# Kernel tuning notes

Measured on AMD Instinct MI355X. Metric: run time of the kernel, lower is better.

Reference implementation:

```python
import jax, jax.numpy as jnp
import numpy as np

# Norse LIFParameters defaults (method='super', alpha=100)
DT = 1e-3
TAU_SYN_INV = 200.0   # 1/5e-3
TAU_MEM_INV = 100.0   # 1/1e-2
V_TH = 1.0
V_LEAK = 0.0
V_RESET = 0.0
ALPHA = 100.0
T = 40                # ConstantCurrentLIFEncoder(40)
SCALE = 50.0
HIDDEN = 64


@jax.custom_vjp
def super_spike(x):
    # Heaviside forward, SuperSpike surrogate gradient backward
    return (x > 0).astype(x.dtype)

def _ss_fwd(x):
    return super_spike(x), x

def _ss_bwd(x, g):
    return (g / (ALPHA * jnp.abs(x) + 1.0) ** 2,)

super_spike.defvjp(_ss_fwd, _ss_bwd)


def encode(current):
    """norse lif_current_encoder unrolled T steps with constant current.
    current: (B, F) -> spikes (T, B, F). Elementwise, so all four encoder
    calls of the original are fused by concatenating along features."""
    def step(v, _):
        v = v + DT * TAU_MEM_INV * ((V_LEAK - v) + current)
        z = super_spike(v - V_TH)
        v = v - z * (v - V_RESET)
        return v, z
    _, spikes = jax.lax.scan(step, jnp.zeros_like(current), None, length=T)
    return spikes


def lif_step(x, z, v, i, w_in, w_rec):
    # norse lif_step semantics
    i_dec = i - DT * TAU_SYN_INV * i
    v_dec = v + DT * TAU_MEM_INV * ((V_LEAK - v) + i)
    z_new = super_spike(v_dec - V_TH)
    v_new = (1.0 - z_new) * v_dec + z_new * V_RESET
    i_new = i_dec + x @ w_in.T + z @ w_rec.T
    return z_new, v_new, i_new


def li_step(x, v, i, w_in):
    # norse li_step (leaky integrator readout)
    i_dec = i - DT * TAU_SYN_INV * i
    v_new = v + DT * TAU_MEM_INV * ((V_LEAK - v) + i)
    i_new = i_dec + x @ w_in.T
    return v_new, i_new


def setup_inputs() -> dict:
    key = jax.random.key(0)
    ks = jax.random.split(key, 9)
    B, S, A = 16384, 24, 4
    def w(k, out_d, in_d):
        return jax.random.normal(k, (out_d, in_d), jnp.float32) * np.sqrt(2.0 / in_d)
    return {
        "state": jax.random.normal(ks[0], (B, S), jnp.float32),
        "action": jax.random.normal(ks[1], (B, A), jnp.float32),
        "W_s_in": w(ks[2], HIDDEN, 2 * S),
        "W_s_rec": w(ks[3], HIDDEN, HIDDEN),
        "W_a_in": w(ks[4], HIDDEN, 2 * A),
        "W_a_rec": w(ks[5], HIDDEN, HIDDEN),
        "W_c_in": w(ks[6], HIDDEN, 2 * HIDDEN),
        "W_c_rec": w(ks[7], HIDDEN, HIDDEN),
        "W_ro": w(ks[8], 1, HIDDEN),
    }


def reference(state, action, W_s_in, W_s_rec, W_a_in, W_a_rec, W_c_in, W_c_rec, W_ro):
    B, S = state.shape
    # constant-current LIF encoding of pos/neg rectified state & action (fused)
    cur = jnp.concatenate([
        jax.nn.relu(SCALE * state), jax.nn.relu(-SCALE * state),
        jax.nn.relu(SCALE * action), jax.nn.relu(-SCALE * action)], axis=1)
    enc = encode(cur)                      # (T, B, 2S+2A)
    state_enc = enc[:, :, :2 * S]          # (T, B, 2S)
    action_enc = enc[:, :, 2 * S:]         # (T, B, 2A)

    z0 = jnp.zeros((B, HIDDEN), state.dtype)
    carry0 = (z0, z0, z0, jnp.zeros((B, 1), state.dtype), jnp.zeros((B, 1), state.dtype))

    def step(carry, xs):
        z, v, i, vli, ili = carry
        xs_s, xs_a = xs
        # NB: original shares one state s0 across all three LIF cells per step
        z_s, v, i = lif_step(xs_s, z, v, i, W_s_in, W_s_rec)
        z_a, v, i = lif_step(xs_a, z_s, v, i, W_a_in, W_a_rec)
        com = jnp.concatenate([z_s, z_a], axis=1)  # (B, 128)
        z, v, i = lif_step(com, z_a, v, i, W_c_in, W_c_rec)
        vli, ili = li_step(z, vli, ili, W_ro)
        return (z, v, i, vli, ili), vli

    _, voltages = jax.lax.scan(step, carry0, (state_enc, action_enc))  # (T, B, 1)
    return jnp.max(voltages, axis=0)  # (B, 1)
```

## Files before the change

kernel.cpp:

```cpp
#include <hip/hip_runtime.h>
#include <stdint.h>


typedef int   i32x4 __attribute__((ext_vector_type(4)));
typedef float f32x4 __attribute__((ext_vector_type(4)));

__launch_bounds__(256)
__attribute__((amdgpu_waves_per_eu(2, 2)))
__global__ void snn_main(const float* __restrict__ state, const float* __restrict__ action,
                         const float* __restrict__ Wsin, const float* __restrict__ Wsrec,
                         const float* __restrict__ Wain, const float* __restrict__ Warec,
                         const float* __restrict__ Wcin, const float* __restrict__ Wcrec,
                         const float* __restrict__ Wro, float* __restrict__ out) {
    __shared__ __align__(16) char smem[32768];

    const int tid  = threadIdx.x;
    const int lane = tid & 63, h = tid >> 6;
    const int l15  = lane & 15, g = lane >> 4;
    const int s    = l15 & 7;

    auto quant = [](float w, int* d) {
        float x = w * 0x1p25f;
        int d3 = __float2int_rn(x * 0x1p-21f); x -= (float)d3 * 0x1p21f;
        int d2 = __float2int_rn(x * 0x1p-14f); x -= (float)d2 * 0x1p14f;
        int d1 = __float2int_rn(x * 0x1p-7f);  x -= (float)d1 * 0x1p7f;
        int d0 = __float2int_rn(x);
        d[0] = d0; d[1] = d1; d[2] = d2; d[3] = d3;
    };
    auto quantMat = [&](auto src) {
        for (int i4 = tid; i4 < 2048; i4 += 256) {
            int base = i4 * 4; int n = base >> 7, k0 = base & 127;
            int sw = n * 128 + ((((k0 >> 4) ^ (n & 7)) << 4) | (k0 & 15));
            uint32_t pk[4] = {0u, 0u, 0u, 0u};
            #pragma unroll
            for (int e = 0; e < 4; ++e) {
                int d[4]; quant(src(n, k0 + e), d);
                #pragma unroll
                for (int p = 0; p < 4; ++p) pk[p] |= (uint32_t)(uint8_t)(char)d[p] << (8 * e);
            }
            #pragma unroll
            for (int p = 0; p < 4; ++p) *(uint32_t*)(smem + p * 8192 + sw) = pk[p];
        }
    };

    const int cS0 = ((g ^ s) << 4);
    const int cS1 = (((4 + g) ^ s) << 4);
    const int i1c = 5 + g;
    const int cC0 = (((1 + g) ^ s) << 4);
    const int cC1 = (((i1c & 8) | ((i1c & 7) ^ s)) << 4);

    i32x4 AS[4][2], AA[4][2], AC[4][2];
    const int arow = (h * 16 + l15) * 128;

    quantMat([&](int n, int k) -> float {
        if (k < 48)  return Wsin[n * 48 + k];
        if (k < 112) return Wsrec[n * 64 + (k - 48)];
        return 0.f;
    });
    __syncthreads();
    #pragma unroll
    for (int p = 0; p < 4; ++p)
    #pragma unroll
    for (int kt = 0; kt < 2; ++kt)
        AS[p][kt] = *(const i32x4*)(smem + p * 8192 + arow + (kt ? cS1 : cS0));
    __syncthreads();

    quantMat([&](int n, int k) -> float {
        float w = Wcin[n * 128 + k];
        if (k >= 64) w += Wcrec[n * 64 + (k - 64)];
        return w;
    });
    __syncthreads();
    #pragma unroll
    for (int p = 0; p < 4; ++p)
    #pragma unroll
    for (int kt = 0; kt < 2; ++kt)
        AC[p][kt] = *(const i32x4*)(smem + p * 8192 + arow + (kt ? cS1 : cS0));
    __syncthreads();

    quantMat([&](int n, int k) -> float {
        if (k < 8)              return Wain[n * 8 + k];
        if (k >= 16 && k < 80)  return Warec[n * 64 + (k - 16)];
        return 0.f;
    });
    __syncthreads();
    #pragma unroll
    for (int p = 0; p < 4; ++p)
    #pragma unroll
    for (int kt = 0; kt < 2; ++kt)
        AA[p][kt] = *(const i32x4*)(smem + p * 8192 + arow + (kt ? cS1 : cS0));
    __syncthreads();

    char*  bS    = smem;
    char*  bAC0  = smem + 2048;
    float* part0 = (float*)(smem + 10240);

    const int ixZs = 1 + h, ixZa = 5 + h, ixZc = 3 + h;
    const int zsOff = l15 * 256 + (((ixZs & 8) | ((ixZs & 7) ^ s)) << 4) + 4 * g;
    const int zaOff = l15 * 256 + (((ixZa & 8) | ((ixZa & 7) ^ s)) << 4) + 4 * g;
    const int zcOff = l15 * 128 + ((ixZc ^ s) << 4) + 4 * g;
    const int encOffS = l15 * 128 + ((h ^ s) << 4) + 4 * g;
    const int encOffA = l15 * 256 + (s << 4) + 4 * g;

    const int rowBase = blockIdx.x * 16;
    const int row = rowBase + l15;

    float cur[4], venc[4];
    #pragma unroll
    for (int e = 0; e < 4; ++e) {
        int f = h * 16 + 4 * g + e;
        float c = 0.f;
        if (f < 24)      c = fmaxf( 50.f * state[row * 24 + f], 0.f);
        else if (f < 48) c = fmaxf(-50.f * state[row * 24 + f - 24], 0.f);
        else if (f < 52) c = fmaxf( 50.f * action[row * 4 + f - 48], 0.f);
        else if (f < 56) c = fmaxf(-50.f * action[row * 4 + f - 52], 0.f);
        cur[e] = c; venc[e] = 0.f;
    }

    float wrof[4];
    #pragma unroll
    for (int r = 0; r < 4; ++r) wrof[r] = Wro[h * 16 + 4 * g + r];

    f32x4 v4 = (f32x4){0.f,0.f,0.f,0.f}, ic4 = (f32x4){0.f,0.f,0.f,0.f};
    bool zc[4] = {false, false, false, false};
    float vli = 0.f, ili = 0.f, vmax = 0.f;

    for (int t = 0; t < 40; ++t) {
        char*  bAC  = bAC0 + ((t & 1) << 12);
        float* part = part0 + ((t & 1) << 6);

        {
            uint32_t zw = (zc[0]?1u:0u)|(zc[1]?0x100u:0u)|(zc[2]?0x10000u:0u)|(zc[3]?0x1000000u:0u);
            *(uint32_t*)(bS + zcOff) = zw;
        }

        f32x4 vd = v4 + 0.1f * (ic4 - v4);
        bool zs[4];
        #pragma unroll
        for (int r = 0; r < 4; ++r) { zs[r] = (vd[r] - 1.0f) > 0.f; if (zs[r]) vd[r] = 0.f; }
        f32x4 vs = vd;
        {
            uint32_t zw = (zs[0]?1u:0u)|(zs[1]?0x100u:0u)|(zs[2]?0x10000u:0u)|(zs[3]?0x1000000u:0u);
            *(uint32_t*)(bAC + zsOff) = zw;
        }

        {
            uint32_t wrd = 0;
            #pragma unroll
            for (int e = 0; e < 4; ++e) {
                float vn = venc[e] + 0.1f * (cur[e] - venc[e]);
                bool sp = (vn - 1.0f) > 0.f;
                venc[e] = sp ? 0.f : vn;
                wrd |= sp ? (1u << (8 * e)) : 0u;
            }
            if (h < 3)          *(uint32_t*)(bS + encOffS) = wrd;
            else if (g < 2)     *(uint32_t*)(bAC + encOffA) = wrd;
        }

        __syncthreads();

        i32x4 acc[4];
        #pragma unroll
        for (int p = 0; p < 4; ++p) acc[p] = (i32x4){0,0,0,0};
        #pragma unroll
        for (int kt = 0; kt < 2; ++kt) {
            i32x4 b = *(const i32x4*)(bS + l15 * 128 + (kt ? cS1 : cS0));
            #pragma unroll
            for (int p = 0; p < 4; ++p)
                acc[p] = __builtin_amdgcn_mfma_i32_16x16x64_i8(AS[p][kt], b, acc[p], 0, 0, 0);
        }
        f32x4 icS;
        {
            i32x4 hi = acc[3] * 128 + acc[2];
            i32x4 lo = acc[1] * 128 + acc[0];
            f32x4 idec = ic4 - 0.2f * ic4;
            #pragma unroll
            for (int r = 0; r < 4; ++r)
                icS[r] = fmaf((float)lo[r], 0x1p-25f, fmaf((float)hi[r], 0x1p-11f, idec[r]));
        }

        vd = vs + 0.1f * (icS - vs);
        bool za[4];
        #pragma unroll
        for (int r = 0; r < 4; ++r) { za[r] = (vd[r] - 1.0f) > 0.f; if (za[r]) vd[r] = 0.f; }
        f32x4 va = vd;
        {
            uint32_t zw = (za[0]?1u:0u)|(za[1]?0x100u:0u)|(za[2]?0x10000u:0u)|(za[3]?0x1000000u:0u);
            *(uint32_t*)(bAC + zaOff) = zw;
        }

        #pragma unroll
        for (int p = 0; p < 4; ++p) acc[p] = (i32x4){0,0,0,0};
        #pragma unroll
        for (int kt = 0; kt < 2; ++kt) {
            i32x4 b = *(const i32x4*)(bAC + l15 * 256 + (kt ? cS1 : cS0));
            #pragma unroll
            for (int p = 0; p < 4; ++p)
                acc[p] = __builtin_amdgcn_mfma_i32_16x16x64_i8(AA[p][kt], b, acc[p], 0, 0, 0);
        }
        f32x4 icA;
        {
            i32x4 hi = acc[3] * 128 + acc[2];
            i32x4 lo = acc[1] * 128 + acc[0];
            f32x4 idec = icS - 0.2f * icS;
            #pragma unroll
            for (int r = 0; r < 4; ++r)
                icA[r] = fmaf((float)lo[r], 0x1p-25f, fmaf((float)hi[r], 0x1p-11f, idec[r]));
        }

        vd = va + 0.1f * (icA - va);
        #pragma unroll
        for (int r = 0; r < 4; ++r) { zc[r] = (vd[r] - 1.0f) > 0.f; if (zc[r]) vd[r] = 0.f; }
        v4 = vd;

        {
            float pr = 0.f;
            #pragma unroll
            for (int r = 0; r < 4; ++r) pr += zc[r] ? wrof[r] : 0.f;
            pr += __shfl_xor(pr, 16);
            pr += __shfl_xor(pr, 32);
            if (g == 0) part[h * 16 + l15] = pr;
        }

        __syncthreads();

        #pragma unroll
        for (int p = 0; p < 4; ++p) acc[p] = (i32x4){0,0,0,0};
        #pragma unroll
        for (int kt = 0; kt < 2; ++kt) {
            i32x4 b = *(const i32x4*)(bAC + l15 * 256 + (kt ? cC1 : cC0));
            #pragma unroll
            for (int p = 0; p < 4; ++p)
                acc[p] = __builtin_amdgcn_mfma_i32_16x16x64_i8(AC[p][kt], b, acc[p], 0, 0, 0);
        }
        {
            i32x4 hi = acc[3] * 128 + acc[2];
            i32x4 lo = acc[1] * 128 + acc[0];
            f32x4 idec = icA - 0.2f * icA;
            #pragma unroll
            for (int r = 0; r < 4; ++r)
                ic4[r] = fmaf((float)lo[r], 0x1p-25f, fmaf((float)hi[r], 0x1p-11f, idec[r]));
        }

        float pt = part[l15] + part[16 + l15] + part[32 + l15] + part[48 + l15];
        float vnew = vli + 0.1f * (ili - vli);
        ili = (ili - 0.2f * ili) + pt;
        vli = vnew;
        vmax = fmaxf(vmax, vli);
    }

    if (h == 0 && g == 0) out[rowBase + l15] = vmax;
}

extern "C" void kernel_launch(void* const* d_in, const int* in_sizes, int n_in,
                              void* d_out, int out_size, void* d_ws, size_t ws_size,
                              hipStream_t stream) {
    const float* state  = (const float*)d_in[0];
    const float* action = (const float*)d_in[1];
    const float* Wsin   = (const float*)d_in[2];
    const float* Wsrec  = (const float*)d_in[3];
    const float* Wain   = (const float*)d_in[4];
    const float* Warec  = (const float*)d_in[5];
    const float* Wcin   = (const float*)d_in[6];
    const float* Wcrec  = (const float*)d_in[7];
    const float* Wro    = (const float*)d_in[8];
    float* out = (float*)d_out;

    const int B = in_sizes[0] / 24;
    snn_main<<<B / 16, 256, 0, stream>>>(state, action, Wsin, Wsrec, Wain, Warec,
                                         Wcin, Wcrec, Wro, out);
}
```

Baseline: 208.2 us.

## Process two 16-row batch groups per block to amortize weight setup and barriers

Each block now handles 32 batch rows as two interleaved 16-row groups. Each group gets its own shared-memory spike buffers and partial-sum slots, and the per-step MFMA chains for the two groups are interleaved. This halves the number of blocks, which amortizes the per-block weight quantization and register loading and halves the barriers per row. The two independent groups also give the MFMA pipeline independent work to overlap. In exchange it raises register pressure under the fixed waves-per-EU setting, doubles shared memory use, and leaves fewer blocks to spread across CUs.

```diff
diff --git a/kernel.cpp b/kernel.cpp
--- a/kernel.cpp
+++ b/kernel.cpp
@@ -91,9 +91,9 @@
         AA[p][kt] = *(const i32x4*)(smem + p * 8192 + arow + (kt ? cS1 : cS0));
     __syncthreads();
 
-    char*  bS    = smem;
-    char*  bAC0  = smem + 2048;
-    float* part0 = (float*)(smem + 10240);
+    char*  bS_[2]  = { smem,        smem + 2048 };
+    char*  bACb[2] = { smem + 4096, smem + 12288 };
+    float* part0   = (float*)(smem + 20480);
 
     const int ixZs = 1 + h, ixZa = 5 + h, ixZc = 3 + h;
     const int zsOff = l15 * 256 + (((ixZs & 8) | ((ixZs & 7) ^ s)) << 4) + 4 * g;
@@ -102,154 +102,170 @@
     const int encOffS = l15 * 128 + ((h ^ s) << 4) + 4 * g;
     const int encOffA = l15 * 256 + (s << 4) + 4 * g;
 
-    const int rowBase = blockIdx.x * 16;
-    const int row = rowBase + l15;
-
-    float cur[4], venc[4];
+    const int rowBase = blockIdx.x * 32;
+
+    float cur[2][4], venc[2][4];
+    #pragma unroll
+    for (int gr = 0; gr < 2; ++gr)
     #pragma unroll
     for (int e = 0; e < 4; ++e) {
         int f = h * 16 + 4 * g + e;
+        int row = rowBase + gr * 16 + l15;
         float c = 0.f;
         if (f < 24)      c = fmaxf( 50.f * state[row * 24 + f], 0.f);
         else if (f < 48) c = fmaxf(-50.f * state[row * 24 + f - 24], 0.f);
         else if (f < 52) c = fmaxf( 50.f * action[row * 4 + f - 48], 0.f);
         else if (f < 56) c = fmaxf(-50.f * action[row * 4 + f - 52], 0.f);
-        cur[e] = c; venc[e] = 0.f;
+        cur[gr][e] = c; venc[gr][e] = 0.f;
     }
 
     float wrof[4];
     #pragma unroll
     for (int r = 0; r < 4; ++r) wrof[r] = Wro[h * 16 + 4 * g + r];
 
-    f32x4 v4 = (f32x4){0.f,0.f,0.f,0.f}, ic4 = (f32x4){0.f,0.f,0.f,0.f};
-    bool zc[4] = {false, false, false, false};
-    float vli = 0.f, ili = 0.f, vmax = 0.f;
+    f32x4 v4[2], ic4[2];
+    bool zc[2][4];
+    float vli[2], ili[2], vmax[2];
+    #pragma unroll
+    for (int gr = 0; gr < 2; ++gr) {
+        v4[gr] = (f32x4){0.f,0.f,0.f,0.f}; ic4[gr] = (f32x4){0.f,0.f,0.f,0.f};
+        vli[gr] = 0.f; ili[gr] = 0.f; vmax[gr] = 0.f;
+        #pragma unroll
+        for (int r = 0; r < 4; ++r) zc[gr][r] = false;
+    }
 
     for (int t = 0; t < 40; ++t) {
-        char*  bAC  = bAC0 + ((t & 1) << 12);
-        float* part = part0 + ((t & 1) << 6);
-
-        {
-            uint32_t zw = (zc[0]?1u:0u)|(zc[1]?0x100u:0u)|(zc[2]?0x10000u:0u)|(zc[3]?0x1000000u:0u);
-            *(uint32_t*)(bS + zcOff) = zw;
-        }
-
-        f32x4 vd = v4 + 0.1f * (ic4 - v4);
-        bool zs[4];
-        #pragma unroll
-        for (int r = 0; r < 4; ++r) { zs[r] = (vd[r] - 1.0f) > 0.f; if (zs[r]) vd[r] = 0.f; }
-        f32x4 vs = vd;
-        {
-            uint32_t zw = (zs[0]?1u:0u)|(zs[1]?0x100u:0u)|(zs[2]?0x10000u:0u)|(zs[3]?0x1000000u:0u);
-            *(uint32_t*)(bAC + zsOff) = zw;
-        }
-
-        {
+        char* bAC[2] = { bACb[0] + ((t & 1) << 12), bACb[1] + ((t & 1) << 12) };
+        float* part  = part0 + ((t & 1) << 7);
+
+        f32x4 vs[2], va[2], icS[2], icA[2];
+        bool zs[2][4], za[2][4];
+
+        #pragma unroll
+        for (int gr = 0; gr < 2; ++gr) {
+            uint32_t zw = (zc[gr][0]?1u:0u)|(zc[gr][1]?0x100u:0u)|(zc[gr][2]?0x10000u:0u)|(zc[gr][3]?0x1000000u:0u);
+            *(uint32_t*)(bS_[gr] + zcOff) = zw;
+
+            f32x4 vd = v4[gr] + 0.1f * (ic4[gr] - v4[gr]);
+            #pragma unroll
+            for (int r = 0; r < 4; ++r) { zs[gr][r] = (vd[r] - 1.0f) > 0.f; if (zs[gr][r]) vd[r] = 0.f; }
+            vs[gr] = vd;
+            uint32_t zw2 = (zs[gr][0]?1u:0u)|(zs[gr][1]?0x100u:0u)|(zs[gr][2]?0x10000u:0u)|(zs[gr][3]?0x1000000u:0u);
+            *(uint32_t*)(bAC[gr] + zsOff) = zw2;
+
             uint32_t wrd = 0;
             #pragma unroll
             for (int e = 0; e < 4; ++e) {
-                float vn = venc[e] + 0.1f * (cur[e] - venc[e]);
+                float vn = venc[gr][e] + 0.1f * (cur[gr][e] - venc[gr][e]);
                 bool sp = (vn - 1.0f) > 0.f;
-                venc[e] = sp ? 0.f : vn;
+                venc[gr][e] = sp ? 0.f : vn;
                 wrd |= sp ? (1u << (8 * e)) : 0u;
             }
-            if (h < 3)          *(uint32_t*)(bS + encOffS) = wrd;
-            else if (g < 2)     *(uint32_t*)(bAC + encOffA) = wrd;
+            if (h < 3)          *(uint32_t*)(bS_[gr] + encOffS) = wrd;
+            else if (g < 2)     *(uint32_t*)(bAC[gr] + encOffA) = wrd;
         }
 
         __syncthreads();
 
-        i32x4 acc[4];
-        #pragma unroll
-        for (int p = 0; p < 4; ++p) acc[p] = (i32x4){0,0,0,0};
-        #pragma unroll
-        for (int kt = 0; kt < 2; ++kt) {
-            i32x4 b = *(const i32x4*)(bS + l15 * 128 + (kt ? cS1 : cS0));
-            #pragma unroll
-            for (int p = 0; p < 4; ++p)
-                acc[p] = __builtin_amdgcn_mfma_i32_16x16x64_i8(AS[p][kt], b, acc[p], 0, 0, 0);
-        }
-        f32x4 icS;
-        {
+        #pragma unroll
+        for (int gr = 0; gr < 2; ++gr) {
+            i32x4 acc[4];
+            #pragma unroll
+            for (int p = 0; p < 4; ++p) acc[p] = (i32x4){0,0,0,0};
+            #pragma unroll
+            for (int kt = 0; kt < 2; ++kt) {
+                i32x4 b = *(const i32x4*)(bS_[gr] + l15 * 128 + (kt ? cS1 : cS0));
+                #pragma unroll
+                for (int p = 0; p < 4; ++p)
+                    acc[p] = __builtin_amdgcn_mfma_i32_16x16x64_i8(AS[p][kt], b, acc[p], 0, 0, 0);
+            }
             i32x4 hi = acc[3] * 128 + acc[2];
             i32x4 lo = acc[1] * 128 + acc[0];
-            f32x4 idec = ic4 - 0.2f * ic4;
+            f32x4 idec = ic4[gr] - 0.2f * ic4[gr];
             #pragma unroll
             for (int r = 0; r < 4; ++r)
-                icS[r] = fmaf((float)lo[r], 0x1p-25f, fmaf((float)hi[r], 0x1p-11f, idec[r]));
-        }
-
-        vd = vs + 0.1f * (icS - vs);
-        bool za[4];
-        #pragma unroll
-        for (int r = 0; r < 4; ++r) { za[r] = (vd[r] - 1.0f) > 0.f; if (za[r]) vd[r] = 0.f; }
-        f32x4 va = vd;
-        {
-            uint32_t zw = (za[0]?1u:0u)|(za[1]?0x100u:0u)|(za[2]?0x10000u:0u)|(za[3]?0x1000000u:0u);
-            *(uint32_t*)(bAC + zaOff) = zw;
-        }
-
-        #pragma unroll
-        for (int p = 0; p < 4; ++p) acc[p] = (i32x4){0,0,0,0};
-        #pragma unroll
-        for (int kt = 0; kt < 2; ++kt) {
-            i32x4 b = *(const i32x4*)(bAC + l15 * 256 + (kt ? cS1 : cS0));
-            #pragma unroll
-            for (int p = 0; p < 4; ++p)
-                acc[p] = __builtin_amdgcn_mfma_i32_16x16x64_i8(AA[p][kt], b, acc[p], 0, 0, 0);
-        }
-        f32x4 icA;
-        {
+                icS[gr][r] = fmaf((float)lo[r], 0x1p-25f, fmaf((float)hi[r], 0x1p-11f, idec[r]));
+        }
+
+        #pragma unroll
+        for (int gr = 0; gr < 2; ++gr) {
+            f32x4 vd = vs[gr] + 0.1f * (icS[gr] - vs[gr]);
+            #pragma unroll
+            for (int r = 0; r < 4; ++r) { za[gr][r] = (vd[r] - 1.0f) > 0.f; if (za[gr][r]) vd[r] = 0.f; }
+            va[gr] = vd;
+            uint32_t zw = (za[gr][0]?1u:0u)|(za[gr][1]?0x100u:0u)|(za[gr][2]?0x10000u:0u)|(za[gr][3]?0x1000000u:0u);
+            *(uint32_t*)(bAC[gr] + zaOff) = zw;
+        }
+
+        #pragma unroll
+        for (int gr = 0; gr < 2; ++gr) {
+            i32x4 acc[4];
+            #pragma unroll
+            for (int p = 0; p < 4; ++p) acc[p] = (i32x4){0,0,0,0};
+            #pragma unroll
+            for (int kt = 0; kt < 2; ++kt) {
+                i32x4 b = *(const i32x4*)(bAC[gr] + l15 * 256 + (kt ? cS1 : cS0));
+                #pragma unroll
+                for (int p = 0; p < 4; ++p)
+                    acc[p] = __builtin_amdgcn_mfma_i32_16x16x64_i8(AA[p][kt], b, acc[p], 0, 0, 0);
+            }
             i32x4 hi = acc[3] * 128 + acc[2];
             i32x4 lo = acc[1] * 128 + acc[0];
-            f32x4 idec = icS - 0.2f * icS;
+            f32x4 idec = icS[gr] - 0.2f * icS[gr];
             #pragma unroll
             for (int r = 0; r < 4; ++r)
-                icA[r] = fmaf((float)lo[r], 0x1p-25f, fmaf((float)hi[r], 0x1p-11f, idec[r]));
-        }
-
-        vd = va + 0.1f * (icA - va);
-        #pragma unroll
-        for (int r = 0; r < 4; ++r) { zc[r] = (vd[r] - 1.0f) > 0.f; if (zc[r]) vd[r] = 0.f; }
-        v4 = vd;
-
-        {
+                icA[gr][r] = fmaf((float)lo[r], 0x1p-25f, fmaf((float)hi[r], 0x1p-11f, idec[r]));
+        }
+
+        #pragma unroll
+        for (int gr = 0; gr < 2; ++gr) {
+            f32x4 vd = va[gr] + 0.1f * (icA[gr] - va[gr]);
+            #pragma unroll
+            for (int r = 0; r < 4; ++r) { zc[gr][r] = (vd[r] - 1.0f) > 0.f; if (zc[gr][r]) vd[r] = 0.f; }
+            v4[gr] = vd;
+
             float pr = 0.f;
             #pragma unroll
-            for (int r = 0; r < 4; ++r) pr += zc[r] ? wrof[r] : 0.f;
+            for (int r = 0; r < 4; ++r) pr += zc[gr][r] ? wrof[r] : 0.f;
             pr += __shfl_xor(pr, 16);
             pr += __shfl_xor(pr, 32);
-            if (g == 0) part[h * 16 + l15] = pr;
+            if (g == 0) part[gr * 64 + h * 16 + l15] = pr;
         }
 
         __syncthreads();
 
         #pragma unroll
-        for (int p = 0; p < 4; ++p) acc[p] = (i32x4){0,0,0,0};
-        #pragma unroll
-        for (int kt = 0; kt < 2; ++kt) {
-            i32x4 b = *(const i32x4*)(bAC + l15 * 256 + (kt ? cC1 : cC0));
-            #pragma unroll
-            for (int p = 0; p < 4; ++p)
-                acc[p] = __builtin_amdgcn_mfma_i32_16x16x64_i8(AC[p][kt], b, acc[p], 0, 0, 0);
-        }
-        {
+        for (int gr = 0; gr < 2; ++gr) {
+            i32x4 acc[4];
+            #pragma unroll
+            for (int p = 0; p < 4; ++p) acc[p] = (i32x4){0,0,0,0};
+            #pragma unroll
+            for (int kt = 0; kt < 2; ++kt) {
+                i32x4 b = *(const i32x4*)(bAC[gr] + l15 * 256 + (kt ? cC1 : cC0));
+                #pragma unroll
+                for (int p = 0; p < 4; ++p)
+                    acc[p] = __builtin_amdgcn_mfma_i32_16x16x64_i8(AC[p][kt], b, acc[p], 0, 0, 0);
+            }
             i32x4 hi = acc[3] * 128 + acc[2];
             i32x4 lo = acc[1] * 128 + acc[0];
-            f32x4 idec = icA - 0.2f * icA;
+            f32x4 idec = icA[gr] - 0.2f * icA[gr];
             #pragma unroll
             for (int r = 0; r < 4; ++r)
-                ic4[r] = fmaf((float)lo[r], 0x1p-25f, fmaf((float)hi[r], 0x1p-11f, idec[r]));
-        }
-
-        float pt = part[l15] + part[16 + l15] + part[32 + l15] + part[48 + l15];
-        float vnew = vli + 0.1f * (ili - vli);
-        ili = (ili - 0.2f * ili) + pt;
-        vli = vnew;
-        vmax = fmaxf(vmax, vli);
-    }
-
-    if (h == 0 && g == 0) out[rowBase + l15] = vmax;
+                ic4[gr][r] = fmaf((float)lo[r], 0x1p-25f, fmaf((float)hi[r], 0x1p-11f, idec[r]));
+
+            float pt = part[gr * 64 + l15] + part[gr * 64 + 16 + l15]
+                     + part[gr * 64 + 32 + l15] + part[gr * 64 + 48 + l15];
+            float vnew = vli[gr] + 0.1f * (ili[gr] - vli[gr]);
+            ili[gr] = (ili[gr] - 0.2f * ili[gr]) + pt;
+            vli[gr] = vnew;
+            vmax[gr] = fmaxf(vmax[gr], vli[gr]);
+        }
+    }
+
+    if (h == 0 && g == 0) {
+        out[rowBase + l15]      = vmax[0];
+        out[rowBase + 16 + l15] = vmax[1];
+    }
 }
 
 extern "C" void kernel_launch(void* const* d_in, const int* in_sizes, int n_in,
@@ -267,6 +283,6 @@
     float* out = (float*)d_out;
 
     const int B = in_sizes[0] / 24;
-    snn_main<<<B / 16, 256, 0, stream>>>(state, action, Wsin, Wsrec, Wain, Warec,
+    snn_main<<<B / 32, 256, 0, stream>>>(state, action, Wsin, Wsrec, Wain, Warec,
                                          Wcin, Wcrec, Wro, out);
 }
```

Result: faster. 182.6 us (-12.3%).
